# Optimization experiments

Measured on AMD Instinct MI355X. Metric: run time of the kernel, lower is better.

Reference implementation:

```python
import jax, jax.numpy as jnp
import numpy as np

B, N, C = 16, 4096, 1024
K = 64
TEMPERATURE = 1.0


def setup_inputs() -> dict:
    key = jax.random.key(0)
    kx, kw = jax.random.split(key)
    x = jax.random.normal(kx, (B, N, C), dtype=jnp.float32)
    # nn.Linear(dim, dim): W is (out, in), b is (out,)
    W = jax.random.normal(kw, (C, C), dtype=jnp.float32) * (1.0 / np.sqrt(C))
    b = jnp.zeros((C,), dtype=jnp.float32)
    return {"x": x, "W": W, "b": b}


def reference(x, W, b):
    Bv, Nv, Cv = x.shape
    # proj = x @ W.T + b ; scores = proj.mean(-1)  -> fold mean into a single matvec:
    # mean(x W^T + b) = x @ (mean of W rows) + mean(b), but keep faithful/explicit form.
    proj = jnp.einsum('bnc,dc->bnd', x, W) + b          # (B, N, C)
    scores = jnp.mean(proj, axis=-1)                    # (B, N)
    k = min(K, Nv)
    _, topk_idx = jax.lax.top_k(scores, k)              # (B, k)
    mask = jnp.zeros_like(scores).at[jnp.arange(Bv)[:, None], topk_idx].set(1.0)
    attn = jax.nn.softmax(scores / TEMPERATURE, axis=-1) * mask  # (B, N)
    out = jnp.einsum('bn,bnc->bc', attn, x)             # (B, C)
    return out, mask
```

## Files before the change

### kernel.cpp

```cpp
#include <hip/hip_runtime.h>
#include <cstdint>

#define B_ 16
#define N_ 4096
#define C_ 1024
#define K_ 64

#define WS_WBAR   0
#define WS_BBAR   1024
#define WS_SCORES 2048
#define WS_TIDX   (WS_SCORES + B_*N_)
#define WS_TATT   (WS_TIDX + B_*K_)
#define WS_PART   (WS_TATT + B_*K_)

__global__ __launch_bounds__(256) void wsum1_kernel(const float* __restrict__ W,
                                                    float* __restrict__ ws) {
    int j = blockIdx.x, t = threadIdx.x;
    const float4* W4 = (const float4*)W;
    float4 s = {0.f, 0.f, 0.f, 0.f};
#pragma unroll
    for (int d = 0; d < 16; ++d) {
        float4 w = W4[(j * 16 + d) * 256 + t];
        s.x += w.x; s.y += w.y; s.z += w.z; s.w += w.w;
    }
    ((float4*)(ws + WS_PART))[j * 256 + t] = s;
}

__global__ __launch_bounds__(256) void wsum2_kernel(const float* __restrict__ b,
                                                    float* __restrict__ ws) {
    int t = threadIdx.x;
    const float4* P4 = (const float4*)(ws + WS_PART);
    float4 s = {0.f, 0.f, 0.f, 0.f};
    for (int j = 0; j < 64; ++j) {
        float4 p = P4[j * 256 + t];
        s.x += p.x; s.y += p.y; s.z += p.z; s.w += p.w;
    }
    const float inv = 1.0f / C_;
    s.x *= inv; s.y *= inv; s.z *= inv; s.w *= inv;
    ((float4*)(ws + WS_WBAR))[t] = s;

    float4 bv = ((const float4*)b)[t];
    float sb = bv.x + bv.y + bv.z + bv.w;
    for (int off = 32; off; off >>= 1) sb += __shfl_xor(sb, off);
    __shared__ float red[4];
    if ((t & 63) == 0) red[t >> 6] = sb;
    __syncthreads();
    if (t == 0) ws[WS_BBAR] = (red[0] + red[1] + red[2] + red[3]) * inv;
}

__global__ __launch_bounds__(512) void scores_kernel(const float* __restrict__ x,
                                                     float* ws) {
    __shared__ float lw[C_];
    int t = threadIdx.x;
    if (t < 256) ((float4*)lw)[t] = ((const float4*)(ws + WS_WBAR))[t];
    __syncthreads();
    int wave = t >> 6, lane = t & 63;
    int row = blockIdx.x * 8 + wave;
    const float4* x4 = (const float4*)x;
    const float4* lw4 = (const float4*)lw;
    float acc = 0.f;
#pragma unroll
    for (int q = 0; q < 4; ++q) {
        float4 xv = x4[row * 256 + q * 64 + lane];
        float4 wv = lw4[q * 64 + lane];
        acc += xv.x * wv.x + xv.y * wv.y + xv.z * wv.z + xv.w * wv.w;
    }
    for (int off = 32; off; off >>= 1) acc += __shfl_xor(acc, off);
    if (lane == 0) ws[WS_SCORES + row] = acc + ws[WS_BBAR];
}

__device__ __forceinline__ unsigned su_(float f) {
    unsigned u = __float_as_uint(f);
    return (u & 0x80000000u) ? ~u : (u | 0x80000000u);
}
__device__ __forceinline__ float isu_(unsigned u) {
    unsigned v = (u & 0x80000000u) ? (u ^ 0x80000000u) : ~u;
    return __uint_as_float(v);
}

__global__ __launch_bounds__(256) void topk_kernel(float* ws,
                                                   float* __restrict__ mask_out) {
    __shared__ unsigned hist[4096];
    __shared__ unsigned long long cand[4096];
    __shared__ float redf[4];
    __shared__ unsigned scnt;
    __shared__ int sbin;
    int b = blockIdx.x, t = threadIdx.x;
    int wid = t >> 6, lane = t & 63;
    const float* srow = ws + WS_SCORES + b * N_;

    float v[16];
#pragma unroll
    for (int e = 0; e < 16; ++e) v[e] = srow[e * 256 + t];

#pragma unroll
    for (int e = 0; e < 16; ++e) hist[e * 256 + t] = 0;
    if (t == 0) scnt = 0;

    float m = v[0];
#pragma unroll
    for (int e = 1; e < 16; ++e) m = fmaxf(m, v[e]);
    for (int off = 32; off; off >>= 1) m = fmaxf(m, __shfl_xor(m, off));
    if (lane == 0) redf[wid] = m;
    __syncthreads();
    m = fmaxf(fmaxf(redf[0], redf[1]), fmaxf(redf[2], redf[3]));

    float dsum = 0.f;
#pragma unroll
    for (int e = 0; e < 16; ++e) dsum += expf(v[e] - m);
    for (int off = 32; off; off >>= 1) dsum += __shfl_xor(dsum, off);

#pragma unroll
    for (int e = 0; e < 16; ++e) atomicAdd(&hist[su_(v[e]) >> 20], 1u);

    __syncthreads();
    if (lane == 0) redf[wid] = dsum;
    __syncthreads();
    float denom = redf[0] + redf[1] + redf[2] + redf[3];

    if (wid == 0) {
        int base = lane * 64;
        unsigned s = 0;
        for (int j = 0; j < 64; ++j) s += hist[base + j];
        unsigned suf = s;
        for (int off = 1; off < 64; off <<= 1) {
            unsigned o = __shfl_down(suf, off);
            if (lane + off < 64) suf += o;
        }
        unsigned above = suf - s;
        if (above < (unsigned)K_ && above + s >= (unsigned)K_) {
            unsigned run = above;
            for (int j = 63; j >= 0; --j) {
                unsigned c = hist[base + j];
                if (run < (unsigned)K_ && run + c >= (unsigned)K_) sbin = base + j;
                run += c;
            }
        }
    }
    __syncthreads();
    int Bn = sbin;

#pragma unroll
    for (int e = 0; e < 16; ++e) {
        unsigned k32 = su_(v[e]);
        if ((int)(k32 >> 20) >= Bn) {
            unsigned p = atomicAdd(&scnt, 1u);
            cand[p] = ((unsigned long long)k32 << 32) |
                      (unsigned long long)(0xFFFFFFFFu - (unsigned)(e * 256 + t));
        }
    }
#pragma unroll
    for (int e = 0; e < 16; ++e) mask_out[b * N_ + e * 256 + t] = 0.0f;
    __syncthreads();

    unsigned mc = scnt;
    int*   tidx = (int*)ws + WS_TIDX;
    float* tatt = ws + WS_TATT;
    for (unsigned i = t; i < mc; i += 256) {
        unsigned long long ki = cand[i];
        unsigned r = 0;
        for (unsigned j = 0; j < mc; ++j) r += (cand[j] > ki) ? 1u : 0u;
        if (r < (unsigned)K_) {
            unsigned widx = 0xFFFFFFFFu - (unsigned)(ki & 0xFFFFFFFFu);
            float sc = isu_((unsigned)(ki >> 32));
            tidx[b * K_ + r] = (int)widx;
            tatt[b * K_ + r] = expf(sc - m) / denom;
            mask_out[b * N_ + widx] = 1.0f;
        }
    }
}

__global__ __launch_bounds__(256) void out_kernel(const float* __restrict__ x,
                                                  const float* __restrict__ ws,
                                                  float* __restrict__ out) {
    int blk = blockIdx.x;
    int b = blk >> 2, cc = blk & 3;
    int t = threadIdx.x;
    __shared__ int   li[K_];
    __shared__ float la[K_];
    if (t < K_) {
        li[t] = ((const int*)ws + WS_TIDX)[b * K_ + t];
        la[t] = (ws + WS_TATT)[b * K_ + t];
    }
    __syncthreads();
    int col = cc * 256 + t;
    float acc = 0.f;
#pragma unroll 8
    for (int r = 0; r < K_; ++r) {
        acc += la[r] * x[(size_t)(b * N_ + li[r]) * C_ + col];
    }
    out[b * C_ + col] = acc;
}

extern "C" void kernel_launch(void* const* d_in, const int* in_sizes, int n_in,
                              void* d_out, int out_size, void* d_ws, size_t ws_size,
                              hipStream_t stream) {
    const float* x = (const float*)d_in[0];
    const float* W = (const float*)d_in[1];
    const float* b = (const float*)d_in[2];
    float* out  = (float*)d_out;
    float* mask = out + B_ * C_;
    float* ws   = (float*)d_ws;

    wsum1_kernel <<<64,           256, 0, stream>>>(W, ws);
    wsum2_kernel <<<1,            256, 0, stream>>>(b, ws);
    scores_kernel<<<B_ * N_ / 8,  512, 0, stream>>>(x, ws);
    topk_kernel  <<<B_,           256, 0, stream>>>(ws, mask);
    out_kernel   <<<B_ * 4,       256, 0, stream>>>(x, ws, out);
}
```

Measured before the change: 67.14 us.

## Fuse top-k with weighted gather, parallelize W reduction, batch score rows per wave

Merges the top-k kernel and the output gather kernel so the selected indices and weights stay in shared memory instead of passing through global workspace, which also removes one launch. The bias mean moves into an extra block of the first W-sum kernel, and the second reduction runs on 4 blocks instead of 1. Each wave in the scores kernel now handles 4 rows for more memory-level parallelism. The cost is that the output gather now runs on only 16 blocks, one per batch, which gives it less parallelism.

```diff
diff --git a/kernel.cpp b/kernel.cpp
--- a/kernel.cpp
+++ b/kernel.cpp
@@ -9,13 +9,22 @@
 #define WS_WBAR   0
 #define WS_BBAR   1024
 #define WS_SCORES 2048
-#define WS_TIDX   (WS_SCORES + B_*N_)
-#define WS_TATT   (WS_TIDX + B_*K_)
-#define WS_PART   (WS_TATT + B_*K_)
+#define WS_PART   (WS_SCORES + B_*N_)
 
 __global__ __launch_bounds__(256) void wsum1_kernel(const float* __restrict__ W,
+                                                    const float* __restrict__ b,
                                                     float* __restrict__ ws) {
     int j = blockIdx.x, t = threadIdx.x;
+    if (j == 64) {
+        float4 bv = ((const float4*)b)[t];
+        float sb = bv.x + bv.y + bv.z + bv.w;
+        for (int off = 32; off; off >>= 1) sb += __shfl_xor(sb, off);
+        __shared__ float red[4];
+        if ((t & 63) == 0) red[t >> 6] = sb;
+        __syncthreads();
+        if (t == 0) ws[WS_BBAR] = (red[0] + red[1] + red[2] + red[3]) * (1.0f / C_);
+        return;
+    }
     const float4* W4 = (const float4*)W;
     float4 s = {0.f, 0.f, 0.f, 0.f};
 #pragma unroll
@@ -26,47 +35,50 @@
     ((float4*)(ws + WS_PART))[j * 256 + t] = s;
 }
 
-__global__ __launch_bounds__(256) void wsum2_kernel(const float* __restrict__ b,
-                                                    float* __restrict__ ws) {
-    int t = threadIdx.x;
-    const float4* P4 = (const float4*)(ws + WS_PART);
-    float4 s = {0.f, 0.f, 0.f, 0.f};
-    for (int j = 0; j < 64; ++j) {
-        float4 p = P4[j * 256 + t];
-        s.x += p.x; s.y += p.y; s.z += p.z; s.w += p.w;
-    }
-    const float inv = 1.0f / C_;
-    s.x *= inv; s.y *= inv; s.z *= inv; s.w *= inv;
-    ((float4*)(ws + WS_WBAR))[t] = s;
-
-    float4 bv = ((const float4*)b)[t];
-    float sb = bv.x + bv.y + bv.z + bv.w;
-    for (int off = 32; off; off >>= 1) sb += __shfl_xor(sb, off);
-    __shared__ float red[4];
-    if ((t & 63) == 0) red[t >> 6] = sb;
-    __syncthreads();
-    if (t == 0) ws[WS_BBAR] = (red[0] + red[1] + red[2] + red[3]) * inv;
+__global__ __launch_bounds__(256) void wsum2_kernel(float* __restrict__ ws) {
+    int col = blockIdx.x * 256 + threadIdx.x;
+    float s = 0.f;
+#pragma unroll 8
+    for (int j = 0; j < 64; ++j) s += ws[WS_PART + j * 1024 + col];
+    ws[WS_WBAR + col] = s * (1.0f / C_);
 }
 
 __global__ __launch_bounds__(512) void scores_kernel(const float* __restrict__ x,
                                                      float* ws) {
     __shared__ float lw[C_];
     int t = threadIdx.x;
+    float bbar = ws[WS_BBAR];
     if (t < 256) ((float4*)lw)[t] = ((const float4*)(ws + WS_WBAR))[t];
     __syncthreads();
     int wave = t >> 6, lane = t & 63;
-    int row = blockIdx.x * 8 + wave;
+    int row0 = blockIdx.x * 32 + wave * 4;
     const float4* x4 = (const float4*)x;
     const float4* lw4 = (const float4*)lw;
-    float acc = 0.f;
+    float a0 = 0.f, a1 = 0.f, a2 = 0.f, a3 = 0.f;
 #pragma unroll
     for (int q = 0; q < 4; ++q) {
-        float4 xv = x4[row * 256 + q * 64 + lane];
         float4 wv = lw4[q * 64 + lane];
-        acc += xv.x * wv.x + xv.y * wv.y + xv.z * wv.z + xv.w * wv.w;
-    }
-    for (int off = 32; off; off >>= 1) acc += __shfl_xor(acc, off);
-    if (lane == 0) ws[WS_SCORES + row] = acc + ws[WS_BBAR];
+        float4 v0 = x4[(row0 + 0) * 256 + q * 64 + lane];
+        float4 v1 = x4[(row0 + 1) * 256 + q * 64 + lane];
+        float4 v2 = x4[(row0 + 2) * 256 + q * 64 + lane];
+        float4 v3 = x4[(row0 + 3) * 256 + q * 64 + lane];
+        a0 += v0.x * wv.x + v0.y * wv.y + v0.z * wv.z + v0.w * wv.w;
+        a1 += v1.x * wv.x + v1.y * wv.y + v1.z * wv.z + v1.w * wv.w;
+        a2 += v2.x * wv.x + v2.y * wv.y + v2.z * wv.z + v2.w * wv.w;
+        a3 += v3.x * wv.x + v3.y * wv.y + v3.z * wv.z + v3.w * wv.w;
+    }
+    for (int off = 32; off; off >>= 1) {
+        a0 += __shfl_xor(a0, off);
+        a1 += __shfl_xor(a1, off);
+        a2 += __shfl_xor(a2, off);
+        a3 += __shfl_xor(a3, off);
+    }
+    if (lane == 0) {
+        ws[WS_SCORES + row0 + 0] = a0 + bbar;
+        ws[WS_SCORES + row0 + 1] = a1 + bbar;
+        ws[WS_SCORES + row0 + 2] = a2 + bbar;
+        ws[WS_SCORES + row0 + 3] = a3 + bbar;
+    }
 }
 
 __device__ __forceinline__ unsigned su_(float f) {
@@ -78,13 +90,17 @@
     return __uint_as_float(v);
 }
 
-__global__ __launch_bounds__(256) void topk_kernel(float* ws,
-                                                   float* __restrict__ mask_out) {
+__global__ __launch_bounds__(256) void topk_out_kernel(const float* __restrict__ x,
+                                                       float* ws,
+                                                       float* __restrict__ out,
+                                                       float* __restrict__ mask_out) {
     __shared__ unsigned hist[4096];
     __shared__ unsigned long long cand[4096];
     __shared__ float redf[4];
     __shared__ unsigned scnt;
     __shared__ int sbin;
+    __shared__ int   li[K_];
+    __shared__ float la[K_];
     int b = blockIdx.x, t = threadIdx.x;
     int wid = t >> 6, lane = t & 63;
     const float* srow = ws + WS_SCORES + b * N_;
@@ -154,8 +170,6 @@
     __syncthreads();
 
     unsigned mc = scnt;
-    int*   tidx = (int*)ws + WS_TIDX;
-    float* tatt = ws + WS_TATT;
     for (unsigned i = t; i < mc; i += 256) {
         unsigned long long ki = cand[i];
         unsigned r = 0;
@@ -163,33 +177,22 @@
         if (r < (unsigned)K_) {
             unsigned widx = 0xFFFFFFFFu - (unsigned)(ki & 0xFFFFFFFFu);
             float sc = isu_((unsigned)(ki >> 32));
-            tidx[b * K_ + r] = (int)widx;
-            tatt[b * K_ + r] = expf(sc - m) / denom;
+            li[r] = (int)widx;
+            la[r] = expf(sc - m) / denom;
             mask_out[b * N_ + widx] = 1.0f;
         }
     }
-}
-
-__global__ __launch_bounds__(256) void out_kernel(const float* __restrict__ x,
-                                                  const float* __restrict__ ws,
-                                                  float* __restrict__ out) {
-    int blk = blockIdx.x;
-    int b = blk >> 2, cc = blk & 3;
-    int t = threadIdx.x;
-    __shared__ int   li[K_];
-    __shared__ float la[K_];
-    if (t < K_) {
-        li[t] = ((const int*)ws + WS_TIDX)[b * K_ + t];
-        la[t] = (ws + WS_TATT)[b * K_ + t];
-    }
-    __syncthreads();
-    int col = cc * 256 + t;
-    float acc = 0.f;
+    __syncthreads();
+
+    const float4* x4 = (const float4*)x;
+    float4 acc = {0.f, 0.f, 0.f, 0.f};
 #pragma unroll 8
     for (int r = 0; r < K_; ++r) {
-        acc += la[r] * x[(size_t)(b * N_ + li[r]) * C_ + col];
-    }
-    out[b * C_ + col] = acc;
+        float a = la[r];
+        float4 xv = x4[(size_t)(b * N_ + li[r]) * 256 + t];
+        acc.x += a * xv.x; acc.y += a * xv.y; acc.z += a * xv.z; acc.w += a * xv.w;
+    }
+    ((float4*)out)[b * 256 + t] = acc;
 }
 
 extern "C" void kernel_launch(void* const* d_in, const int* in_sizes, int n_in,
@@ -202,9 +205,8 @@
     float* mask = out + B_ * C_;
     float* ws   = (float*)d_ws;
 
-    wsum1_kernel <<<64,           256, 0, stream>>>(W, ws);
-    wsum2_kernel <<<1,            256, 0, stream>>>(b, ws);
-    scores_kernel<<<B_ * N_ / 8,  512, 0, stream>>>(x, ws);
-    topk_kernel  <<<B_,           256, 0, stream>>>(ws, mask);
-    out_kernel   <<<B_ * 4,       256, 0, stream>>>(x, ws, out);
-}
+    wsum1_kernel   <<<65,          256, 0, stream>>>(W, b, ws);
+    wsum2_kernel   <<<4,           256, 0, stream>>>(ws);
+    scores_kernel  <<<B_ * N_ / 32, 512, 0, stream>>>(x, ws);
+    topk_out_kernel<<<B_,          256, 0, stream>>>(x, ws, out, mask);
+}
```

Result: slower. 70.44 us (+4.9%).
